# Performance work log

Hardware: AMD Instinct MI355X
Metric: run time of the kernel (lower is better)

Reference implementation:

```python
import jax, jax.numpy as jnp
import numpy as np

NUM_ENT, NUM_REL, D, B, FEW, NN, STEPS = 100000, 5000, 100, 256, 3, 200, 4
DM = 2 * D    # 200 = d_model
DI = 2 * DM   # 400 = FFN inner / LSTM hidden


def setup_inputs() -> dict:
    key = jax.random.key(0)
    ks = jax.random.split(key, 40)
    f = lambda i, sh: jax.random.normal(ks[i], sh, dtype=jnp.float32) * 0.1
    ri = lambda i, sh, hi: jax.random.randint(ks[i], sh, 0, hi, dtype=jnp.int32)
    z = lambda n: jnp.zeros((n,), jnp.float32)
    inp = dict(
        ent_emb=f(0, (NUM_ENT, D)), rel_emb=f(1, (NUM_REL, D)),
        W1=f(2, (D, D)), b1=z(D), W2=f(3, (D, D)), b2=z(D), W3=f(4, (D, D)), b3=z(D),
        attW1=f(5, (DM, 1)), attb1=z(1), attW2=f(6, (DM, 1)), attb2=z(1),
        seW1=f(7, (DM, DI)), seb1=z(DI), seW2=f(8, (DI, DM)), seb2=z(DM),
        ln_g=jnp.ones((DM,), jnp.float32), ln_b=z(DM),
        Wih=f(9, (DM, 4 * DI)), bih=z(4 * DI), Whh=f(10, (DI, 4 * DI)), bhh=z(4 * DI),
        query=ri(11, (B, 2), NUM_ENT), support=ri(12, (FEW, 2), NUM_ENT),
        qlc_out=ri(13, (B, NN, 2), NUM_REL), qlc_in=ri(14, (B, NN, 2), NUM_REL),
        qld=ri(15, (B,), NN),
        qrc_out=ri(16, (B, NN, 2), NUM_REL), qrc_in=ri(17, (B, NN, 2), NUM_REL),
        qrd=ri(18, (B,), NN),
        slc_out=ri(19, (FEW, NN, 2), NUM_REL), slc_in=ri(20, (FEW, NN, 2), NUM_REL),
        sld=ri(21, (FEW,), NN),
        src_out=ri(22, (FEW, NN, 2), NUM_REL), src_in=ri(23, (FEW, NN, 2), NUM_REL),
        srd=ri(24, (FEW,), NN),
    )
    return inp


def reference(ent_emb, rel_emb, W1, b1, W2, b2, W3, b3, attW1, attb1, attW2, attb2,
              seW1, seb1, seW2, seb2, ln_g, ln_b, Wih, bih, Whh, bhh,
              query, support, qlc_out, qlc_in, qld, qrc_out, qrc_in, qrd,
              slc_out, slc_in, sld, src_out, src_in, srd):
    # 3 L2-normalized linear 'views' of every embedding  -> (N, 3, D)
    def nrm(x):
        n = jnp.sqrt(jnp.sum(x * x, axis=1, keepdims=True))
        return x / jnp.maximum(n, 1e-12)
    views = lambda e: jnp.stack([nrm(e @ W1 + b1), nrm(e @ W2 + b2), nrm(e @ W3 + b3)], axis=1)
    ent_v = views(ent_emb)   # (NUM_ENT, 3, D)
    rel_v = views(rel_emb)   # (NUM_REL, 3, D)

    def neigh(left, right, c_out, c_in):
        # c_*: (b, n, 2) int; col0 = relation id, col1 = entity id
        rel_out = rel_v[c_out[:, :, 0]]  # (b, n, 3, D)
        ent_out = ent_v[c_out[:, :, 1]]
        rel_in = rel_v[c_in[:, :, 0]]
        ent_in = ent_v[c_in[:, :, 1]]
        rr = (ent_v[right] - ent_v[left])[:, None]        # (b, 1, 3, D)
        rr = jnp.broadcast_to(rr, rel_out.shape)
        a_in = jax.nn.softmax(jnp.concatenate([rel_in, rr], -1) @ attW1 + attb1, axis=1)
        a_out = jax.nn.softmax(jnp.concatenate([rel_out, rr], -1) @ attW2 + attb2, axis=1)
        h_in = jnp.sum(a_in * ent_in, axis=1)             # (b, 3, D)
        h_out = jnp.sum(a_out * ent_out, axis=1)
        e_in, e_out = jnp.exp(h_in), jnp.exp(h_out)
        return jnp.tanh((h_in * e_in + h_out * e_out) / (e_in + e_out))

    def senc(x):  # residual FFN + layernorm over last dim
        h = jax.nn.relu(x @ seW1 + seb1) @ seW2 + seb2 + x
        mu = h.mean(-1, keepdims=True)
        var = ((h - mu) ** 2).mean(-1, keepdims=True)
        return ln_g * (h - mu) / jnp.sqrt(var + 1e-5) + ln_b

    def qenc(supp, q):  # matching-network process block; supp: (3, DM), q: (b, DM)
        h_r = jnp.zeros((q.shape[0], 2 * DM), q.dtype)
        c = jnp.zeros_like(h_r)
        def step(carry, _):
            h_r, c = carry
            gates = q @ Wih + bih + h_r @ Whh + bhh
            i, fg, g, o = jnp.split(gates, 4, axis=-1)
            c2 = jax.nn.sigmoid(fg) * c + jax.nn.sigmoid(i) * jnp.tanh(g)
            h2 = jax.nn.sigmoid(o) * jnp.tanh(c2)
            h = q + h2[:, :DM]
            r = jax.nn.softmax(h @ supp.T, axis=1) @ supp
            return (jnp.concatenate([h, r], -1), c2), None
        (h_r, c), _ = jax.lax.scan(step, (h_r, c), None, length=STEPS)
        return h_r[:, :DM]

    ql = neigh(query[:, 0], query[:, 1], qlc_out, qlc_in)
    qr = neigh(query[:, 0], query[:, 1], qrc_out, qrc_in)
    sl = neigh(support[:, 0], support[:, 1], slc_out, slc_in)
    sr = neigh(support[:, 0], support[:, 1], src_out, src_in)
    qn = jnp.concatenate([ql, qr], -1)   # (B, 3, 2D)
    sn = jnp.concatenate([sl, sr], -1)   # (FEW, 3, 2D)
    sg = senc(sn).mean(0, keepdims=True)  # (1, 3, DM)
    qg = senc(qn)                          # (B, 3, DM)
    supp = sg[0]                           # (3, DM)
    s1 = (qenc(supp, qg[:, 0]) @ sg[:, 0].T)[:, 0]
    s2 = (qenc(supp, qg[:, 1]) @ sg[:, 1].T)[:, 0]
    s3 = (qenc(supp, qg[:, 2]) @ sg[:, 2].T)[:, 0]
    return jnp.maximum(jnp.maximum(s1, s2), s3)
```

## Files before the change

### kernel.cpp

```cpp
#include <hip/hip_runtime.h>
#include <math.h>

#define D_    100
#define DM_   200
#define DI_   400
#define G4_   1600
#define NN_   200
#define KP_   224

typedef __attribute__((ext_vector_type(8))) short bf16x8;
typedef __attribute__((ext_vector_type(4))) float f32x4;

__device__ __forceinline__ float sigf(float x){ return 1.0f/(1.0f+__expf(-x)); }
__device__ __forceinline__ unsigned short f2bf(float f){
    unsigned int b = __float_as_uint(f);
    b = (b + 0x7fffu + ((b>>16)&1u)) >> 16;
    return (unsigned short)b;
}
__device__ __forceinline__ float bf_lo(unsigned int w){ return __uint_as_float(w<<16); }
__device__ __forceinline__ float bf_hi(unsigned int w){ return __uint_as_float(w & 0xffff0000u); }

__global__ __launch_bounds__(256) void warm_kernel(
    const float4* __restrict__ p0, int n0, const float4* __restrict__ p1, int n1,
    const float4* __restrict__ p2, int n2, const float4* __restrict__ p3, int n3,
    const float4* __restrict__ p4, int n4, float* __restrict__ dump)
{
    int tid = threadIdx.x, bid = blockIdx.x;
    int total = n0 + n1 + n2 + n3 + n4;
    int nsl = gridDim.x >> 3;
    int slice = bid >> 3;
    int chunk = (total + nsl - 1) / nsl;
    int start = slice * chunk;
    int end = min(start + chunk, total);
    float acc = 0.f;
    for (int i = start + tid; i < end; i += 256){
        int j = i; const float4* p;
        if (j < n0) p = p0;
        else { j -= n0;
            if (j < n1) p = p1;
            else { j -= n1;
                if (j < n2) p = p2;
                else { j -= n2;
                    if (j < n3) p = p3;
                    else { j -= n3; p = p4; } } } }
        float4 v = p[j];
        acc += v.x + v.y + v.z + v.w;
    }
    #pragma unroll
    for (int o = 32; o; o >>= 1) acc += __shfl_down(acc, o);
    if ((tid & 63) == 0) dump[bid*4 + (tid >> 6)] = acc;
}

__global__ __launch_bounds__(128) void views_kernel(
    const float* __restrict__ ent_emb, const float* __restrict__ rel_emb,
    const float* __restrict__ W1, const float* __restrict__ b1,
    const float* __restrict__ W2, const float* __restrict__ b2,
    const float* __restrict__ W3, const float* __restrict__ b3,
    const float* __restrict__ attW1, const float* __restrict__ attW2,
    unsigned short* __restrict__ ent_bf, float* __restrict__ rs_in, float* __restrict__ rs_out)
{
    int bid = blockIdx.x, tid = threadIdx.x;
    bool isRel = bid < 625;
    int row0 = (isRel ? bid : bid - 625) * 8;
    const float* src = isRel ? rel_emb : ent_emb;

    __shared__ float4 eT4[25][9];
    __shared__ float  ys[3][8][D_];
    __shared__ float  invn[3][8];
    __shared__ float  aws[2][D_];

    for (int idx = tid; idx < 200; idx += 128){
        int r = idx / 25, c4 = idx % 25;
        eT4[c4][r] = *(const float4*)(src + (long)(row0+r)*D_ + c4*4);
    }
    if (isRel){
        for (int idx = tid; idx < 200; idx += 128)
            aws[idx/100][idx%100] = (idx < 100) ? attW1[idx] : attW2[idx-100];
    }
    __syncthreads();

    if (tid < 75){
        int v = tid / 25, cq = tid % 25, c0 = cq*4;
        const float* Wv = (v==0) ? W1 : (v==1) ? W2 : W3;
        const float* bv = (v==0) ? b1 : (v==1) ? b2 : b3;
        float4 bb = *(const float4*)(bv + c0);
        float acc[8][4];
        #pragma unroll
        for (int r = 0; r < 8; ++r){
            acc[r][0]=bb.x; acc[r][1]=bb.y; acc[r][2]=bb.z; acc[r][3]=bb.w;
        }
        for (int k4 = 0; k4 < 25; ++k4){
            const float* Wk = Wv + (long)(k4*4)*D_ + c0;
            float4 w0 = *(const float4*)(Wk);
            float4 w1 = *(const float4*)(Wk + D_);
            float4 w2 = *(const float4*)(Wk + 2*D_);
            float4 w3 = *(const float4*)(Wk + 3*D_);
            #pragma unroll
            for (int r = 0; r < 8; ++r){
                float4 e = eT4[k4][r];
                acc[r][0] += e.x*w0.x + e.y*w1.x + e.z*w2.x + e.w*w3.x;
                acc[r][1] += e.x*w0.y + e.y*w1.y + e.z*w2.y + e.w*w3.y;
                acc[r][2] += e.x*w0.z + e.y*w1.z + e.z*w2.z + e.w*w3.z;
                acc[r][3] += e.x*w0.w + e.y*w1.w + e.z*w2.w + e.w*w3.w;
            }
        }
        #pragma unroll
        for (int r = 0; r < 8; ++r)
            *(float4*)(&ys[v][r][c0]) = make_float4(acc[r][0], acc[r][1], acc[r][2], acc[r][3]);
    }
    __syncthreads();

    if (tid < 24){
        int v = tid / 8, r = tid % 8;
        float s = 0.f;
        #pragma unroll 4
        for (int j = 0; j < D_; ++j){ float t = ys[v][r][j]; s += t*t; }
        invn[v][r] = 1.f / fmaxf(sqrtf(s), 1e-12f);
    }
    __syncthreads();

    if (isRel){
        if (tid < 48){
            int which = tid & 1, p = tid >> 1;
            int v = p / 8, r = p % 8;
            float s = 0.f;
            #pragma unroll 4
            for (int j = 0; j < D_; ++j) s += ys[v][r][j]*aws[which][j];
            (which ? rs_out : rs_in)[(row0+r)*3+v] = s * invn[v][r];
        }
    } else {
        for (int idx = tid; idx < 600; idx += 128){
            int v = idx / 200, rq = idx - v*200;
            int r = rq / 25, c0 = (rq % 25)*4;
            float inv = invn[v][r];
            float4 y4 = *(const float4*)(&ys[v][r][c0]);
            ushort4 o;
            o.x = f2bf(y4.x*inv); o.y = f2bf(y4.y*inv);
            o.z = f2bf(y4.z*inv); o.w = f2bf(y4.w*inv);
            *(ushort4*)(ent_bf + ((long)(row0+r)*3+v)*D_ + c0) = o;
        }
    }
}

__global__ __launch_bounds__(512) void neigh_kernel(
    const int* __restrict__ qlc_out, const int* __restrict__ qlc_in,
    const int* __restrict__ qrc_out, const int* __restrict__ qrc_in,
    const int* __restrict__ slc_out, const int* __restrict__ slc_in,
    const int* __restrict__ src_out, const int* __restrict__ src_in,
    const unsigned short* __restrict__ ent_bf, const float* __restrict__ rs_in,
    const float* __restrict__ rs_out,
    float* __restrict__ X)
{
    int u = blockIdx.x, v = blockIdx.y, tid = threadIdx.x;
    const int *cin, *cout; int row, colOff;
    if      (u < 256){ int n=u;     cout=qlc_out+n*NN_*2; cin=qlc_in+n*NN_*2; row=v*256+n;   colOff=0;   }
    else if (u < 512){ int n=u-256; cout=qrc_out+n*NN_*2; cin=qrc_in+n*NN_*2; row=v*256+n;   colOff=100; }
    else if (u < 515){ int f=u-512; cout=slc_out+f*NN_*2; cin=slc_in+f*NN_*2; row=768+f*3+v; colOff=0;   }
    else             { int f=u-515; cout=src_out+f*NN_*2; cin=src_in+f*NN_*2; row=768+f*3+v; colOff=100; }

    __shared__ int   ioff[NN_], ooff[NN_];
    __shared__ float ain[NN_], aout[NN_];
    __shared__ float sv[2][NN_];
    __shared__ float red[512];
    __shared__ float pin[4][D_], pout[4][D_];

    if (tid < NN_){
        int rrel = cin[tid*2], rent = cin[tid*2+1];
        ioff[tid] = (rent*3+v)*D_;
        sv[0][tid] = rs_in[rrel*3+v];
    } else if (tid >= 256 && tid < 256+NN_){
        int k = tid - 256;
        int rrel = cout[k*2], rent = cout[k*2+1];
        ooff[k] = (rent*3+v)*D_;
        sv[1][k] = rs_out[rrel*3+v];
    }
    __syncthreads();

    int half = tid >> 8, l = tid & 255, base = half << 8;
    float x = (l < NN_) ? sv[half][l] : -1e30f;
    red[tid] = x; __syncthreads();
    for (int s = 128; s > 0; s >>= 1){
        if (l < s) red[base+l] = fmaxf(red[base+l], red[base+l+s]);
        __syncthreads();
    }
    float m = red[base]; __syncthreads();
    float e = (l < NN_) ? __expf(x - m) : 0.f;
    red[tid] = e; __syncthreads();
    for (int s = 128; s > 0; s >>= 1){
        if (l < s) red[base+l] += red[base+l+s];
        __syncthreads();
    }
    float S = red[base];
    if (l < NN_){ if (half) aout[l] = e/S; else ain[l] = e/S; }
    __syncthreads();

    int g = tid >> 6, ln = tid & 63;
    if (ln < 50){
        int d0 = ln*2;
        bool isOut = g >= 4;
        int k0 = (g & 3) * 50;
        const int*   offA = isOut ? ooff : ioff;
        const float* aA   = isOut ? aout : ain;
        float acc0 = 0.f, acc1 = 0.f;
        #pragma unroll 5
        for (int kk = 0; kk < 50; ++kk){
            int k = k0 + kk;
            unsigned int w = *(const unsigned int*)(ent_bf + offA[k] + d0);
            float a = aA[k];
            acc0 += a * bf_lo(w);
            acc1 += a * bf_hi(w);
        }
        float2* p = isOut ? (float2*)&pout[g&3][d0] : (float2*)&pin[g&3][d0];
        *p = make_float2(acc0, acc1);
    }
    __syncthreads();

    if (tid < D_){
        float hi = pin[0][tid]+pin[1][tid]+pin[2][tid]+pin[3][tid];
        float ho = pout[0][tid]+pout[1][tid]+pout[2][tid]+pout[3][tid];
        float ea = __expf(hi), ec = __expf(ho);
        X[(long)row*DM_ + colOff + tid] = tanhf((hi*ea + ho*ec)/(ea+ec));
    }
}

__global__ __launch_bounds__(512) void senc_kernel(
    const float* __restrict__ X,
    const float* __restrict__ seW1, const float* __restrict__ seb1,
    const float* __restrict__ seW2, const float* __restrict__ seb2,
    const float* __restrict__ ln_g, const float* __restrict__ ln_b,
    float* __restrict__ qg, float* __restrict__ sEnc)
{
    int b = blockIdx.x, tid = threadIdx.x;
    int r0 = b*2;

    __shared__ float xT[DM_][2];
    __shared__ float tT[DI_][2];
    __shared__ float pc[2][DM_][2];
    __shared__ float hv[2][DM_];
    __shared__ float part[2][4][2];

    for (int idx = tid; idx < 400; idx += 512){
        int r = idx / DM_, k = idx - r*DM_;
        int row = r0 + r;
        xT[k][r] = (row < 777) ? X[(long)row*DM_ + k] : 0.f;
    }
    __syncthreads();

    if (tid < DI_){
        int col = tid;
        float a0, a1; a0 = a1 = seb1[col];
        #pragma unroll 4
        for (int k = 0; k < DM_; ++k){
            float w = seW1[(long)k*DI_ + col];
            float2 e = *(const float2*)(&xT[k][0]);
            a0 += e.x*w; a1 += e.y*w;
        }
        tT[col][0] = fmaxf(a0, 0.f);
        tT[col][1] = fmaxf(a1, 0.f);
    }
    __syncthreads();

    if (tid < 400){
        int col = tid % DM_, kh = tid / DM_;
        float a0 = 0.f, a1 = 0.f;
        #pragma unroll 4
        for (int kk = 0; kk < 200; ++kk){
            int k = kh*200 + kk;
            float w = seW2[(long)k*DM_ + col];
            float2 t = *(const float2*)(&tT[k][0]);
            a0 += t.x*w; a1 += t.y*w;
        }
        pc[kh][col][0] = a0; pc[kh][col][1] = a1;
    }
    __syncthreads();

    if (tid < DM_){
        int col = tid;
        float bb = seb2[col];
        hv[0][col] = pc[0][col][0] + pc[1][col][0] + bb + xT[col][0];
        hv[1][col] = pc[0][col][1] + pc[1][col][1] + bb + xT[col][1];
    }
    __syncthreads();

    {
        int row = tid >> 8, l = tid & 255, w = l >> 6, lane = l & 63;
        float v = (l < DM_) ? hv[row][l] : 0.f;
        float s1 = v, s2 = v*v;
        #pragma unroll
        for (int o = 32; o; o >>= 1){ s1 += __shfl_down(s1, o); s2 += __shfl_down(s2, o); }
        if (lane == 0){ part[row][w][0] = s1; part[row][w][1] = s2; }
    }
    __syncthreads();

    if (tid < 400){
        int row = tid / DM_, col = tid % DM_;
        int grow = r0 + row;
        if (grow < 777){
            float s1 = part[row][0][0]+part[row][1][0]+part[row][2][0]+part[row][3][0];
            float s2 = part[row][0][1]+part[row][1][1]+part[row][2][1]+part[row][3][1];
            float mu = s1 * (1.f/DM_);
            float rs = rsqrtf(s2 * (1.f/DM_) - mu*mu + 1e-5f);
            float* out = (grow < 768) ? qg + (long)grow*DM_ : sEnc + (long)(grow-768)*DM_;
            out[col] = ln_g[col]*(hv[row][col]-mu)*rs + ln_b[col];
        }
    }
}

__global__ __launch_bounds__(256) void wtrans_kernel(
    const float* __restrict__ Wih, const float* __restrict__ Whh,
    unsigned short* __restrict__ Bt0, unsigned short* __restrict__ Bt1)
{
    int b = blockIdx.x;
    int m = b / 175; b -= m*175;
    int kt = b / 25, ct = b % 25;
    const float* W = m ? Whh : Wih;
    unsigned short* Bt = m ? Bt1 : Bt0;
    int k0 = kt*32, c0 = ct*64;
    int tid = threadIdx.x;
    __shared__ float t[32][65];
    for (int idx = tid; idx < 2048; idx += 256){
        int kk = idx >> 6, c = idx & 63;
        int k = k0 + kk;
        t[kk][c] = (k < 200) ? W[(long)k*G4_ + c0 + c] : 0.f;
    }
    __syncthreads();
    for (int idx = tid; idx < 1024; idx += 256){
        int c = idx >> 4, p = idx & 15;
        unsigned int u0 = f2bf(t[p*2][c]);
        unsigned int u1 = f2bf(t[p*2+1][c]);
        *(unsigned int*)(Bt + (long)(c0+c)*KP_ + k0 + p*2) = u0 | (u1 << 16);
    }
}

__global__ __launch_bounds__(64) void aconv_kernel(
    const float* __restrict__ qg, unsigned short* __restrict__ Abf)
{
    int row = blockIdx.x, l = threadIdx.x;
    const float* q = qg + (long)row*DM_;
    unsigned short* o = Abf + (long)row*KP_;
    o[l]      = f2bf(q[l]);
    o[l+64]   = f2bf(q[l+64]);
    o[l+128]  = f2bf(q[l+128]);
    if (l < 8)  o[l+192] = f2bf(q[l+192]);
    if (l < 24) o[l+200] = 0;
}

__global__ __launch_bounds__(64) void sw_kernel(
    const float* __restrict__ sEnc, const float* __restrict__ Whh,
    float* __restrict__ sg, float* __restrict__ sW)
{
    int b = blockIdx.x, tid = threadIdx.x;
    int s = b / 25, c0 = (b - s*25)*64;
    __shared__ float sgl[DM_];
    for (int j = tid; j < DM_; j += 64){
        float val = (sEnc[s*DM_ + j] + sEnc[(3+s)*DM_ + j] + sEnc[(6+s)*DM_ + j]) * (1.f/3.f);
        sgl[j] = val;
        if (c0 == 0) sg[s*DM_ + j] = val;
    }
    __syncthreads();
    int col = c0 + tid;
    float acc = 0.f;
    #pragma unroll 4
    for (int i = 0; i < DM_; ++i) acc += sgl[i] * Whh[(long)(DM_+i)*G4_ + col];
    sW[s*G4_ + col] = acc;
}

__global__ __launch_bounds__(256) void gemm_mfma_kernel(
    const unsigned short* __restrict__ Abf, const unsigned short* __restrict__ Bt,
    const float* __restrict__ qW0, const float* __restrict__ sW,
    const float* __restrict__ alpha,
    const float* __restrict__ bih, const float* __restrict__ bhh,
    float* __restrict__ C, int mode)
{
    int bx = blockIdx.x % 25, by = blockIdx.x / 25;
    int tid = threadIdx.x;
    int w = tid >> 6, lane = tid & 63;
    int row0 = by*16;
    int col0 = bx*64 + w*16;
    int kg = (lane >> 4) * 8;

    const unsigned short* Ap = Abf + (long)(row0 + (lane & 15))*KP_ + kg;
    const unsigned short* Bp = Bt  + (long)(col0 + (lane & 15))*KP_ + kg;

    f32x4 acc = {0.f, 0.f, 0.f, 0.f};
    #pragma unroll
    for (int kt = 0; kt < 7; ++kt){
        bf16x8 a = *(const bf16x8*)(Ap + kt*32);
        bf16x8 b = *(const bf16x8*)(Bp + kt*32);
        acc = __builtin_amdgcn_mfma_f32_16x16x32_bf16(a, b, acc, 0, 0, 0);
    }

    int crow0 = row0 + (lane >> 4)*4;
    int ccol  = col0 + (lane & 15);
    if (mode == 0){
        float add = bih[ccol] + bhh[ccol];
        #pragma unroll
        for (int i = 0; i < 4; ++i)
            C[(long)(crow0+i)*G4_ + ccol] = acc[i] + add;
    } else {
        float s0 = sW[ccol], s1 = sW[G4_ + ccol], s2 = sW[2*G4_ + ccol];
        #pragma unroll
        for (int i = 0; i < 4; ++i){
            int row = crow0 + i;
            float a0 = alpha[row*3+0], a1 = alpha[row*3+1], a2 = alpha[row*3+2];
            C[(long)row*G4_ + ccol] = acc[i] + qW0[(long)row*G4_ + ccol]
                                    + a0*s0 + a1*s1 + a2*s2;
        }
    }
}

__global__ __launch_bounds__(256) void cell_kernel(
    const float* __restrict__ G, const float* __restrict__ qg,
    const float* __restrict__ sg, float* __restrict__ c,
    float* __restrict__ h, unsigned short* __restrict__ hbf,
    float* __restrict__ alpha, float* __restrict__ sAll,
    int first, int last)
{
    int b = blockIdx.x, tid = threadIdx.x;
    int row0 = b*4;
    __shared__ float hbuf[4][DM_];
    __shared__ float sup[600];
    __shared__ float lg[4][3];

    for (int i = tid; i < 600; i += 256) sup[i] = sg[i];

    for (int idx = tid; idx < 4*DI_; idx += 256){
        int r = idx / DI_, j = idx - r*DI_;
        int row = row0 + r;
        const float* g = G + (long)row*G4_;
        float gi = g[j], gf = g[DI_+j], gg = g[2*DI_+j];
        float cold = first ? 0.f : c[(long)row*DI_ + j];
        float c2 = sigf(gf)*cold + sigf(gi)*tanhf(gg);
        c[(long)row*DI_ + j] = c2;
        if (j < DM_){
            float go = g[3*DI_+j];
            float hval = qg[(long)row*DM_ + j] + sigf(go)*tanhf(c2);
            hbuf[r][j] = hval;
            h[(long)row*DM_ + j] = hval;
            hbf[(long)row*KP_ + j] = f2bf(hval);
        }
    }
    __syncthreads();

    if (!last){
        if (tid < 192){
            int p = tid >> 4, l = tid & 15, r = p/3, s = p - r*3;
            float part = 0.f;
            for (int d = l; d < DM_; d += 16) part += hbuf[r][d]*sup[s*DM_+d];
            for (int o = 8; o; o >>= 1) part += __shfl_down(part, o, 16);
            if (!l) lg[r][s] = part;
        }
        __syncthreads();
        if (tid < 4){
            float l0 = lg[tid][0], l1 = lg[tid][1], l2 = lg[tid][2];
            float m = fmaxf(l0, fmaxf(l1, l2));
            float e0 = __expf(l0-m), e1 = __expf(l1-m), e2 = __expf(l2-m);
            float inv = 1.f/(e0+e1+e2);
            alpha[(row0+tid)*3+0] = e0*inv;
            alpha[(row0+tid)*3+1] = e1*inv;
            alpha[(row0+tid)*3+2] = e2*inv;
        }
    } else {
        int v = row0 >> 8;
        if (tid < 64){
            int r = tid >> 4, l = tid & 15;
            float part = 0.f;
            for (int d = l; d < DM_; d += 16) part += hbuf[r][d]*sup[v*DM_+d];
            for (int o = 8; o; o >>= 1) part += __shfl_down(part, o, 16);
            if (!l) sAll[row0+r] = part;
        }
    }
}

__global__ void final_kernel(const float* __restrict__ sAll, float* __restrict__ out){
    int n = blockIdx.x*blockDim.x + threadIdx.x;
    if (n < 256) out[n] = fmaxf(sAll[n], fmaxf(sAll[256+n], sAll[512+n]));
}

extern "C" void kernel_launch(void* const* d_in, const int* in_sizes, int n_in,
                              void* d_out, int out_size, void* d_ws, size_t ws_size,
                              hipStream_t stream)
{
    const float* ent_emb=(const float*)d_in[0];
    const float* rel_emb=(const float*)d_in[1];
    const float* W1=(const float*)d_in[2];  const float* b1=(const float*)d_in[3];
    const float* W2=(const float*)d_in[4];  const float* b2=(const float*)d_in[5];
    const float* W3=(const float*)d_in[6];  const float* b3=(const float*)d_in[7];
    const float* attW1=(const float*)d_in[8];
    const float* attW2=(const float*)d_in[10];
    const float* seW1=(const float*)d_in[12]; const float* seb1=(const float*)d_in[13];
    const float* seW2=(const float*)d_in[14]; const float* seb2=(const float*)d_in[15];
    const float* ln_g=(const float*)d_in[16]; const float* ln_b=(const float*)d_in[17];
    const float* Wih=(const float*)d_in[18];  const float* bih=(const float*)d_in[19];
    const float* Whh=(const float*)d_in[20];  const float* bhh=(const float*)d_in[21];
    const int* qlc_out=(const int*)d_in[24];  const int* qlc_in=(const int*)d_in[25];
    const int* qrc_out=(const int*)d_in[27];  const int* qrc_in=(const int*)d_in[28];
    const int* slc_out=(const int*)d_in[30];  const int* slc_in=(const int*)d_in[31];
    const int* src_out=(const int*)d_in[33];  const int* src_in=(const int*)d_in[34];

    float* ws = (float*)d_ws;
    unsigned short* ent_bf = (unsigned short*)ws;
    float* gates = ws;
    float* rs_in = ws + 1500000;
    float* rs_out= ws + 1515000;
    float* X     = ws + 1530000;
    float* qg    = ws + 1686800;
    float* sEnc  = ws + 1840400;
    float* sg    = ws + 1842200;
    float* qW0   = ws + 1842800;
    float* cst   = ws + 3071600;
    float* alpha = ws + 3378800;
    float* sW    = ws + 3381104;
    float* sAll  = ws + 3385904;
    float* dump  = ws + 3386672;
    unsigned short* Abf = (unsigned short*)(ws + 3394864);
    unsigned short* Bt0 = (unsigned short*)(ws + 3480880);
    unsigned short* Bt1 = (unsigned short*)(ws + 3660080);
    float* h     = X;

    warm_kernel<<<2048, 256, 0, stream>>>(
        (const float4*)ent_emb, 125000, (const float4*)rel_emb, 125000,
        (const float4*)W1, 2500, (const float4*)W2, 2500,
        (const float4*)W3, 2500, dump);
    views_kernel<<<1250, 128, 0, stream>>>(ent_emb, rel_emb, W1,b1,W2,b2,W3,b3,
                                           attW1, attW2, ent_bf, rs_in, rs_out);
    neigh_kernel<<<dim3(518,3), 512, 0, stream>>>(qlc_out,qlc_in,qrc_out,qrc_in,
                                                  slc_out,slc_in,src_out,src_in,
                                                  ent_bf, rs_in, rs_out, X);
    wtrans_kernel<<<350, 256, 0, stream>>>(Wih, Whh, Bt0, Bt1);
    warm_kernel<<<512, 256, 0, stream>>>(
        (const float4*)(Whh + 200*G4_), 80000, (const float4*)seW1, 0,
        (const float4*)seW1, 0, (const float4*)seW1, 0,
        (const float4*)seW1, 0, dump);
    warm_kernel<<<512, 256, 0, stream>>>(
        (const float4*)seW1, 20000, (const float4*)seW2, 20000,
        (const float4*)seW1, 0, (const float4*)seW1, 0,
        (const float4*)seW1, 0, dump);
    senc_kernel<<<389, 512, 0, stream>>>(X, seW1, seb1, seW2, seb2,
                                         ln_g, ln_b, qg, sEnc);
    aconv_kernel<<<768, 64, 0, stream>>>(qg, Abf);
    sw_kernel<<<75, 64, 0, stream>>>(sEnc, Whh, sg, sW);

    gemm_mfma_kernel<<<1200, 256, 0, stream>>>(Abf, Bt0, nullptr, nullptr, nullptr,
                                               bih, bhh, qW0, 0);
    cell_kernel<<<192, 256, 0, stream>>>(qW0, qg, sg, cst, h, Abf, alpha, sAll, 1, 0);
    for (int s = 1; s < 4; ++s){
        gemm_mfma_kernel<<<1200, 256, 0, stream>>>(Abf, Bt1, qW0, sW, alpha,
                                                   nullptr, nullptr, gates, 1);
        cell_kernel<<<192, 256, 0, stream>>>(gates, qg, sg, cst, h, Abf, alpha, sAll,
                                             0, (s==3) ? 1 : 0);
    }
    final_kernel<<<1, 256, 0, stream>>>(sAll, (float*)d_out);
}
```

Baseline: 154.3 us.

## Fuse LSTM gemm and cell steps into one persistent kernel; merge prep kernels

Replaces the four gemm/cell kernel pairs of the LSTM loop with one kernel in which each block owns 16 query rows. The block keeps the cell state, hidden state and softmax weights in LDS across all four steps and computes the i/f/g/o gates for the same columns together. The weight transpose and warm-up launches are merged into a single prep kernel, and the bf16 conversion of qg is folded into the senc epilogue. This removes about ten launches and the global round trips for gates, cell state and alpha. In exchange only 48 blocks run, so far fewer CUs are in use and each block reads all of Bt from global/L2 on every step.

```diff
diff --git a/kernel.cpp b/kernel.cpp
--- a/kernel.cpp
+++ b/kernel.cpp
@@ -51,6 +51,57 @@
     if ((tid & 63) == 0) dump[bid*4 + (tid >> 6)] = acc;
 }
 
+__global__ __launch_bounds__(256) void prep_kernel(
+    const float* __restrict__ Wih, const float* __restrict__ Whh,
+    const float* __restrict__ seW1, const float* __restrict__ seW2,
+    unsigned short* __restrict__ Bt0, unsigned short* __restrict__ Bt1,
+    float* __restrict__ dump)
+{
+    int b = blockIdx.x, tid = threadIdx.x;
+    if (b < 350){
+        int m = b / 175; int bb = b - m*175;
+        int kt = bb / 25, ct = bb % 25;
+        const float* W = m ? Whh : Wih;
+        unsigned short* Bt = m ? Bt1 : Bt0;
+        int k0 = kt*32, c0 = ct*64;
+        __shared__ float t[32][65];
+        for (int idx = tid; idx < 2048; idx += 256){
+            int kk = idx >> 6, c = idx & 63;
+            int k = k0 + kk;
+            t[kk][c] = (k < 200) ? W[(long)k*G4_ + c0 + c] : 0.f;
+        }
+        __syncthreads();
+        for (int idx = tid; idx < 1024; idx += 256){
+            int c = idx >> 4, p = idx & 15;
+            unsigned int u0 = f2bf(t[p*2][c]);
+            unsigned int u1 = f2bf(t[p*2+1][c]);
+            *(unsigned int*)(Bt + (long)(c0+c)*KP_ + k0 + p*2) = u0 | (u1 << 16);
+        }
+        return;
+    }
+    const float4* p; int total; int sub;
+    if (b < 862){ sub = b - 350; p = (const float4*)(Whh + 200*G4_); total = 80000; }
+    else        { sub = b - 862; p = (const float4*)seW1;            total = 40000; }
+    int nsl = 64, slice = sub >> 3;
+    int chunk = (total + nsl - 1) / nsl;
+    int start = slice * chunk;
+    int end = min(start + chunk, total);
+    float acc = 0.f;
+    if (b < 862){
+        for (int i = start + tid; i < end; i += 256){ float4 v = p[i]; acc += v.x+v.y+v.z+v.w; }
+    } else {
+        const float4* q1 = (const float4*)seW1;
+        const float4* q2 = (const float4*)seW2;
+        for (int i = start + tid; i < end; i += 256){
+            float4 v = (i < 20000) ? q1[i] : q2[i-20000];
+            acc += v.x+v.y+v.z+v.w;
+        }
+    }
+    #pragma unroll
+    for (int o = 32; o; o >>= 1) acc += __shfl_down(acc, o);
+    if ((tid & 63) == 0) dump[b*4 + (tid >> 6)] = acc;
+}
+
 __global__ __launch_bounds__(128) void views_kernel(
     const float* __restrict__ ent_emb, const float* __restrict__ rel_emb,
     const float* __restrict__ W1, const float* __restrict__ b1,
@@ -228,7 +279,8 @@
     const float* __restrict__ seW1, const float* __restrict__ seb1,
     const float* __restrict__ seW2, const float* __restrict__ seb2,
     const float* __restrict__ ln_g, const float* __restrict__ ln_b,
-    float* __restrict__ qg, float* __restrict__ sEnc)
+    float* __restrict__ qg, float* __restrict__ sEnc,
+    unsigned short* __restrict__ Abf)
 {
     int b = blockIdx.x, tid = threadIdx.x;
     int r0 = b*2;
@@ -300,49 +352,20 @@
             float s2 = part[row][0][1]+part[row][1][1]+part[row][2][1]+part[row][3][1];
             float mu = s1 * (1.f/DM_);
             float rs = rsqrtf(s2 * (1.f/DM_) - mu*mu + 1e-5f);
-            float* out = (grow < 768) ? qg + (long)grow*DM_ : sEnc + (long)(grow-768)*DM_;
-            out[col] = ln_g[col]*(hv[row][col]-mu)*rs + ln_b[col];
-        }
-    }
-}
-
-__global__ __launch_bounds__(256) void wtrans_kernel(
-    const float* __restrict__ Wih, const float* __restrict__ Whh,
-    unsigned short* __restrict__ Bt0, unsigned short* __restrict__ Bt1)
-{
-    int b = blockIdx.x;
-    int m = b / 175; b -= m*175;
-    int kt = b / 25, ct = b % 25;
-    const float* W = m ? Whh : Wih;
-    unsigned short* Bt = m ? Bt1 : Bt0;
-    int k0 = kt*32, c0 = ct*64;
-    int tid = threadIdx.x;
-    __shared__ float t[32][65];
-    for (int idx = tid; idx < 2048; idx += 256){
-        int kk = idx >> 6, c = idx & 63;
-        int k = k0 + kk;
-        t[kk][c] = (k < 200) ? W[(long)k*G4_ + c0 + c] : 0.f;
-    }
-    __syncthreads();
-    for (int idx = tid; idx < 1024; idx += 256){
-        int c = idx >> 4, p = idx & 15;
-        unsigned int u0 = f2bf(t[p*2][c]);
-        unsigned int u1 = f2bf(t[p*2+1][c]);
-        *(unsigned int*)(Bt + (long)(c0+c)*KP_ + k0 + p*2) = u0 | (u1 << 16);
-    }
-}
-
-__global__ __launch_bounds__(64) void aconv_kernel(
-    const float* __restrict__ qg, unsigned short* __restrict__ Abf)
-{
-    int row = blockIdx.x, l = threadIdx.x;
-    const float* q = qg + (long)row*DM_;
-    unsigned short* o = Abf + (long)row*KP_;
-    o[l]      = f2bf(q[l]);
-    o[l+64]   = f2bf(q[l+64]);
-    o[l+128]  = f2bf(q[l+128]);
-    if (l < 8)  o[l+192] = f2bf(q[l+192]);
-    if (l < 24) o[l+200] = 0;
+            float val = ln_g[col]*(hv[row][col]-mu)*rs + ln_b[col];
+            if (grow < 768){
+                qg[(long)grow*DM_ + col] = val;
+                Abf[(long)grow*KP_ + col] = f2bf(val);
+            } else {
+                sEnc[(long)(grow-768)*DM_ + col] = val;
+            }
+        }
+    } else if (tid < 448){
+        int t = tid - 400;
+        int rr = t / 24, cc = t % 24;
+        int grow = r0 + rr;
+        if (grow < 768) Abf[(long)grow*KP_ + 200 + cc] = 0;
+    }
 }
 
 __global__ __launch_bounds__(64) void sw_kernel(
@@ -365,107 +388,125 @@
     sW[s*G4_ + col] = acc;
 }
 
-__global__ __launch_bounds__(256) void gemm_mfma_kernel(
-    const unsigned short* __restrict__ Abf, const unsigned short* __restrict__ Bt,
-    const float* __restrict__ qW0, const float* __restrict__ sW,
-    const float* __restrict__ alpha,
-    const float* __restrict__ bih, const float* __restrict__ bhh,
-    float* __restrict__ C, int mode)
-{
-    int bx = blockIdx.x % 25, by = blockIdx.x / 25;
-    int tid = threadIdx.x;
-    int w = tid >> 6, lane = tid & 63;
-    int row0 = by*16;
-    int col0 = bx*64 + w*16;
+__global__ __launch_bounds__(256) void lstm_kernel(
+    const unsigned short* __restrict__ Abf,
+    const unsigned short* __restrict__ Bt0, const unsigned short* __restrict__ Bt1,
+    const float* __restrict__ qg, const float* __restrict__ sg,
+    const float* __restrict__ sW, const float* __restrict__ bih,
+    const float* __restrict__ bhh,
+    float* __restrict__ qW0, float* __restrict__ sAll)
+{
+    int b = blockIdx.x, tid = threadIdx.x;
+    int row0 = b*16;
+    int lane = tid & 63, w = tid >> 6;
+    int cr = lane & 15;
     int kg = (lane >> 4) * 8;
 
-    const unsigned short* Ap = Abf + (long)(row0 + (lane & 15))*KP_ + kg;
-    const unsigned short* Bp = Bt  + (long)(col0 + (lane & 15))*KP_ + kg;
-
-    f32x4 acc = {0.f, 0.f, 0.f, 0.f};
-    #pragma unroll
-    for (int kt = 0; kt < 7; ++kt){
-        bf16x8 a = *(const bf16x8*)(Ap + kt*32);
-        bf16x8 b = *(const bf16x8*)(Bp + kt*32);
-        acc = __builtin_amdgcn_mfma_f32_16x16x32_bf16(a, b, acc, 0, 0, 0);
-    }
-
-    int crow0 = row0 + (lane >> 4)*4;
-    int ccol  = col0 + (lane & 15);
-    if (mode == 0){
-        float add = bih[ccol] + bhh[ccol];
+    __shared__ unsigned short A_lds[16][232];
+    __shared__ float cst[16][404];
+    __shared__ float hbuf[16][204];
+    __shared__ float qgl[16][200];
+    __shared__ float sup[600];
+    __shared__ float alf[16][3];
+    __shared__ float lg[16][3];
+
+    for (int idx = tid; idx < 448; idx += 256){
+        int r = idx / 28, c = idx % 28;
+        *(uint4*)(&A_lds[r][c*8]) = *(const uint4*)(Abf + (long)(row0+r)*KP_ + c*8);
+    }
+    for (int idx = tid; idx < 800; idx += 256){
+        int r = idx / 50, c = idx % 50;
+        *(float4*)(&qgl[r][c*4]) = *(const float4*)(qg + (long)(row0+r)*DM_ + c*4);
+    }
+    for (int idx = tid; idx < 600; idx += 256) sup[idx] = sg[idx];
+    for (int idx = tid; idx < 16*404; idx += 256) (&cst[0][0])[idx] = 0.f;
+    __syncthreads();
+
+    for (int step = 0; step < 4; ++step){
+        const unsigned short* Bt = step ? Bt1 : Bt0;
+        bf16x8 a[7];
         #pragma unroll
-        for (int i = 0; i < 4; ++i)
-            C[(long)(crow0+i)*G4_ + ccol] = acc[i] + add;
-    } else {
-        float s0 = sW[ccol], s1 = sW[G4_ + ccol], s2 = sW[2*G4_ + ccol];
-        #pragma unroll
-        for (int i = 0; i < 4; ++i){
-            int row = crow0 + i;
-            float a0 = alpha[row*3+0], a1 = alpha[row*3+1], a2 = alpha[row*3+2];
-            C[(long)row*G4_ + ccol] = acc[i] + qW0[(long)row*G4_ + ccol]
-                                    + a0*s0 + a1*s1 + a2*s2;
-        }
-    }
-}
-
-__global__ __launch_bounds__(256) void cell_kernel(
-    const float* __restrict__ G, const float* __restrict__ qg,
-    const float* __restrict__ sg, float* __restrict__ c,
-    float* __restrict__ h, unsigned short* __restrict__ hbf,
-    float* __restrict__ alpha, float* __restrict__ sAll,
-    int first, int last)
-{
-    int b = blockIdx.x, tid = threadIdx.x;
-    int row0 = b*4;
-    __shared__ float hbuf[4][DM_];
-    __shared__ float sup[600];
-    __shared__ float lg[4][3];
-
-    for (int i = tid; i < 600; i += 256) sup[i] = sg[i];
-
-    for (int idx = tid; idx < 4*DI_; idx += 256){
-        int r = idx / DI_, j = idx - r*DI_;
-        int row = row0 + r;
-        const float* g = G + (long)row*G4_;
-        float gi = g[j], gf = g[DI_+j], gg = g[2*DI_+j];
-        float cold = first ? 0.f : c[(long)row*DI_ + j];
-        float c2 = sigf(gf)*cold + sigf(gi)*tanhf(gg);
-        c[(long)row*DI_ + j] = c2;
-        if (j < DM_){
-            float go = g[3*DI_+j];
-            float hval = qg[(long)row*DM_ + j] + sigf(go)*tanhf(c2);
-            hbuf[r][j] = hval;
-            h[(long)row*DM_ + j] = hval;
-            hbf[(long)row*KP_ + j] = f2bf(hval);
-        }
-    }
-    __syncthreads();
-
-    if (!last){
-        if (tid < 192){
-            int p = tid >> 4, l = tid & 15, r = p/3, s = p - r*3;
-            float part = 0.f;
-            for (int d = l; d < DM_; d += 16) part += hbuf[r][d]*sup[s*DM_+d];
-            for (int o = 8; o; o >>= 1) part += __shfl_down(part, o, 16);
-            if (!l) lg[r][s] = part;
-        }
+        for (int kt = 0; kt < 7; ++kt)
+            a[kt] = *(const bf16x8*)(&A_lds[cr][kg + kt*32]);
         __syncthreads();
-        if (tid < 4){
-            float l0 = lg[tid][0], l1 = lg[tid][1], l2 = lg[tid][2];
-            float m = fmaxf(l0, fmaxf(l1, l2));
-            float e0 = __expf(l0-m), e1 = __expf(l1-m), e2 = __expf(l2-m);
-            float inv = 1.f/(e0+e1+e2);
-            alpha[(row0+tid)*3+0] = e0*inv;
-            alpha[(row0+tid)*3+1] = e1*inv;
-            alpha[(row0+tid)*3+2] = e2*inv;
-        }
-    } else {
-        int v = row0 >> 8;
-        if (tid < 64){
+
+        for (int tj = w; tj < 25; tj += 4){
+            int jc = tj*16 + cr;
+            const unsigned short* BI = Bt + (long)(jc       )*KP_ + kg;
+            const unsigned short* BF = Bt + (long)(jc +  400)*KP_ + kg;
+            const unsigned short* BG = Bt + (long)(jc +  800)*KP_ + kg;
+            const unsigned short* BO = Bt + (long)(jc + 1200)*KP_ + kg;
+            f32x4 ai = {0,0,0,0}, af = {0,0,0,0}, ag = {0,0,0,0}, ao = {0,0,0,0};
+            #pragma unroll
+            for (int kt = 0; kt < 7; ++kt){
+                ai = __builtin_amdgcn_mfma_f32_16x16x32_bf16(a[kt], *(const bf16x8*)(BI + kt*32), ai, 0, 0, 0);
+                af = __builtin_amdgcn_mfma_f32_16x16x32_bf16(a[kt], *(const bf16x8*)(BF + kt*32), af, 0, 0, 0);
+                ag = __builtin_amdgcn_mfma_f32_16x16x32_bf16(a[kt], *(const bf16x8*)(BG + kt*32), ag, 0, 0, 0);
+                ao = __builtin_amdgcn_mfma_f32_16x16x32_bf16(a[kt], *(const bf16x8*)(BO + kt*32), ao, 0, 0, 0);
+            }
+            float addI = 0.f, addF = 0.f, addG = 0.f, addO = 0.f;
+            if (step == 0){
+                addI = bih[jc]      + bhh[jc];
+                addF = bih[400+jc]  + bhh[400+jc];
+                addG = bih[800+jc]  + bhh[800+jc];
+                addO = bih[1200+jc] + bhh[1200+jc];
+            }
+            #pragma unroll
+            for (int i = 0; i < 4; ++i){
+                int rl = (lane >> 4)*4 + i;
+                int grow = row0 + rl;
+                float gi, gf, gg, go;
+                if (step == 0){
+                    gi = ai[i] + addI; gf = af[i] + addF;
+                    gg = ag[i] + addG; go = ao[i] + addO;
+                    float* qp = qW0 + (long)grow*G4_;
+                    qp[jc] = gi; qp[400+jc] = gf; qp[800+jc] = gg; qp[1200+jc] = go;
+                } else {
+                    float A0 = alf[rl][0], A1 = alf[rl][1], A2 = alf[rl][2];
+                    const float* qp = qW0 + (long)grow*G4_;
+                    gi = ai[i] + qp[jc]       + A0*sW[jc]        + A1*sW[1600+jc]      + A2*sW[3200+jc];
+                    gf = af[i] + qp[400+jc]   + A0*sW[400+jc]    + A1*sW[2000+jc]      + A2*sW[3600+jc];
+                    gg = ag[i] + qp[800+jc]   + A0*sW[800+jc]    + A1*sW[2400+jc]      + A2*sW[4000+jc];
+                    go = ao[i] + qp[1200+jc]  + A0*sW[1200+jc]   + A1*sW[2800+jc]      + A2*sW[4400+jc];
+                }
+                float cold = cst[rl][jc];
+                float c2 = sigf(gf)*cold + sigf(gi)*tanhf(gg);
+                cst[rl][jc] = c2;
+                float h2 = sigf(go)*tanhf(c2);
+                if (jc < DM_){
+                    float hval = qgl[rl][jc] + h2;
+                    hbuf[rl][jc] = hval;
+                    A_lds[rl][jc] = f2bf(hval);
+                }
+            }
+        }
+        __syncthreads();
+
+        if (step < 3){
+            int r = tid >> 4, l = tid & 15;
+            #pragma unroll
+            for (int s = 0; s < 3; ++s){
+                float part = 0.f;
+                for (int d = l; d < DM_; d += 16) part += hbuf[r][d]*sup[s*DM_+d];
+                #pragma unroll
+                for (int o = 8; o; o >>= 1) part += __shfl_down(part, o, 16);
+                if (!l) lg[r][s] = part;
+            }
+            __syncthreads();
+            if (tid < 16){
+                float l0 = lg[tid][0], l1 = lg[tid][1], l2 = lg[tid][2];
+                float m = fmaxf(l0, fmaxf(l1, l2));
+                float e0 = __expf(l0-m), e1 = __expf(l1-m), e2 = __expf(l2-m);
+                float inv = 1.f/(e0+e1+e2);
+                alf[tid][0] = e0*inv; alf[tid][1] = e1*inv; alf[tid][2] = e2*inv;
+            }
+            __syncthreads();
+        } else {
+            int v = b >> 4;
             int r = tid >> 4, l = tid & 15;
             float part = 0.f;
             for (int d = l; d < DM_; d += 16) part += hbuf[r][d]*sup[v*DM_+d];
+            #pragma unroll
             for (int o = 8; o; o >>= 1) part += __shfl_down(part, o, 16);
             if (!l) sAll[row0+r] = part;
         }
@@ -500,7 +541,6 @@
 
     float* ws = (float*)d_ws;
     unsigned short* ent_bf = (unsigned short*)ws;
-    float* gates = ws;
     float* rs_in = ws + 1500000;
     float* rs_out= ws + 1515000;
     float* X     = ws + 1530000;
@@ -508,15 +548,12 @@
     float* sEnc  = ws + 1840400;
     float* sg    = ws + 1842200;
     float* qW0   = ws + 1842800;
-    float* cst   = ws + 3071600;
-    float* alpha = ws + 3378800;
     float* sW    = ws + 3381104;
     float* sAll  = ws + 3385904;
     float* dump  = ws + 3386672;
     unsigned short* Abf = (unsigned short*)(ws + 3394864);
     unsigned short* Bt0 = (unsigned short*)(ws + 3480880);
     unsigned short* Bt1 = (unsigned short*)(ws + 3660080);
-    float* h     = X;
 
     warm_kernel<<<2048, 256, 0, stream>>>(
         (const float4*)ent_emb, 125000, (const float4*)rel_emb, 125000,
@@ -527,28 +564,11 @@
     neigh_kernel<<<dim3(518,3), 512, 0, stream>>>(qlc_out,qlc_in,qrc_out,qrc_in,
                                                   slc_out,slc_in,src_out,src_in,
                                                   ent_bf, rs_in, rs_out, X);
-    wtrans_kernel<<<350, 256, 0, stream>>>(Wih, Whh, Bt0, Bt1);
-    warm_kernel<<<512, 256, 0, stream>>>(
-        (const float4*)(Whh + 200*G4_), 80000, (const float4*)seW1, 0,
-        (const float4*)seW1, 0, (const float4*)seW1, 0,
-        (const float4*)seW1, 0, dump);
-    warm_kernel<<<512, 256, 0, stream>>>(
-        (const float4*)seW1, 20000, (const float4*)seW2, 20000,
-        (const float4*)seW1, 0, (const float4*)seW1, 0,
-        (const float4*)seW1, 0, dump);
+    prep_kernel<<<1374, 256, 0, stream>>>(Wih, Whh, seW1, seW2, Bt0, Bt1, dump);
     senc_kernel<<<389, 512, 0, stream>>>(X, seW1, seb1, seW2, seb2,
-                                         ln_g, ln_b, qg, sEnc);
-    aconv_kernel<<<768, 64, 0, stream>>>(qg, Abf);
+                                         ln_g, ln_b, qg, sEnc, Abf);
     sw_kernel<<<75, 64, 0, stream>>>(sEnc, Whh, sg, sW);
-
-    gemm_mfma_kernel<<<1200, 256, 0, stream>>>(Abf, Bt0, nullptr, nullptr, nullptr,
-                                               bih, bhh, qW0, 0);
-    cell_kernel<<<192, 256, 0, stream>>>(qW0, qg, sg, cst, h, Abf, alpha, sAll, 1, 0);
-    for (int s = 1; s < 4; ++s){
-        gemm_mfma_kernel<<<1200, 256, 0, stream>>>(Abf, Bt1, qW0, sW, alpha,
-                                                   nullptr, nullptr, gates, 1);
-        cell_kernel<<<192, 256, 0, stream>>>(gates, qg, sg, cst, h, Abf, alpha, sAll,
-                                             0, (s==3) ? 1 : 0);
-    }
+    lstm_kernel<<<48, 256, 0, stream>>>(Abf, Bt0, Bt1, qg, sg, sW, bih, bhh,
+                                        qW0, sAll);
     final_kernel<<<1, 256, 0, stream>>>(sAll, (float*)d_out);
 }
```

Result: slower. 202.4 us (+31.1%).
